# Kernel tuning notes

Hardware: AMD Instinct MI355X
Metric: run time of the kernel (lower is better)

## Reference

```python
import jax, jax.numpy as jnp
import numpy as np

B, S, D, H = 2, 2048, 1024, 16
DH = D // H  # 64


def setup_inputs() -> dict:
    key = jax.random.key(0)
    ks = jax.random.split(key, 6)
    scale = 1.0 / np.sqrt(D)
    x = jax.random.normal(ks[0], (B, S, D), dtype=jnp.float32)
    Wq = jax.random.normal(ks[1], (D, D), dtype=jnp.float32) * scale
    Wk = jax.random.normal(ks[2], (D, D), dtype=jnp.float32) * scale
    Wv = jax.random.normal(ks[3], (D, D), dtype=jnp.float32) * scale
    Wo = jax.random.normal(ks[4], (D, D), dtype=jnp.float32) * scale
    zeros = jnp.zeros((D,), dtype=jnp.float32)
    return {"x": x, "Wq": Wq, "bq": zeros, "Wk": Wk, "bk": zeros,
            "Wv": Wv, "bv": zeros, "Wo": Wo, "bo": zeros}


def reference(x, Wq, bq, Wk, bk, Wv, bv, Wo, bo):
    # x: [B, S, D]
    def split_heads(t):
        # [B, S, D] -> [B, H, S, DH]
        return t.reshape(B, S, H, DH).transpose(0, 2, 1, 3)

    q = split_heads(x @ Wq + bq)
    k = split_heads(x @ Wk + bk)
    v = split_heads(x @ Wv + bv)

    scores = jnp.einsum('bhqd,bhkd->bhqk', q, k) / jnp.sqrt(jnp.float32(DH))
    weights = jax.nn.softmax(scores, axis=-1)          # [B, H, S, S]
    o = jnp.einsum('bhqk,bhkd->bhqd', weights, v)       # [B, H, S, DH]
    o = o.transpose(0, 2, 1, 3).reshape(B, S, D)        # merge heads
    return o @ Wo + bo
```

## Files before the change

kernel.cpp:

```cpp
#include <hip/hip_runtime.h>
#include <hip/hip_bf16.h>

#define DEV __device__ __forceinline__

typedef short bf16x8 __attribute__((ext_vector_type(8)));
typedef float f32x4 __attribute__((ext_vector_type(4)));
typedef unsigned int u32;

constexpr int BB = 2, SS = 2048, DD = 1024, HH = 16, DHD = 64;
constexpr int MM = BB * SS;
#define QSC 0.1803368801111f

#if __has_builtin(__builtin_amdgcn_exp2f)
#define EXP2(x) __builtin_amdgcn_exp2f(x)
#else
#define EXP2(x) exp2f(x)
#endif

DEV unsigned short f2bf(float f) {
    union { float f; unsigned int u; } v; v.f = f;
    return (unsigned short)((v.u + 0x8000u) >> 16);
}
DEV u32 pk2bf(float a, float b) {
    union { float f; u32 u; } ua, ub; ua.f = a; ub.f = b;
    return ((ua.u + 0x8000u) >> 16) | ((ub.u + 0x8000u) & 0xffff0000u);
}

DEV bf16x8 ld_bf16x8(const unsigned short* p) { return *(const bf16x8*)p; }

DEV void gl16(const unsigned short* g, unsigned short* l) {
    __builtin_amdgcn_global_load_lds(
        (const __attribute__((address_space(1))) u32*)g,
        (__attribute__((address_space(3))) u32*)l, 16, 0, 0);
}

__global__ void x2bf(const float* __restrict__ x, unsigned short* __restrict__ xb) {
    int i = blockIdx.x * 256 + threadIdx.x;
    float4 v = ((const float4*)x)[i];
    uint2 o;
    o.x = pk2bf(v.x, v.y);
    o.y = pk2bf(v.z, v.w);
    ((uint2*)xb)[i] = o;
}

__global__ void transpose_w4(const float* __restrict__ W0, const float* __restrict__ W1,
                             const float* __restrict__ W2, const float* __restrict__ W3,
                             unsigned short* __restrict__ WtBase) {
    __shared__ float tile[32][33];
    const float* W = (blockIdx.z == 0) ? W0 : (blockIdx.z == 1) ? W1 : (blockIdx.z == 2) ? W2 : W3;
    unsigned short* Wt = WtBase + (size_t)blockIdx.z * DD * DD;
    int n0 = blockIdx.x * 32, k0 = blockIdx.y * 32;
    int tx = threadIdx.x, ty = threadIdx.y;
    #pragma unroll
    for (int i = 0; i < 4; ++i)
        tile[ty + 8 * i][tx] = W[(size_t)(k0 + ty + 8 * i) * DD + n0 + tx];
    __syncthreads();
    #pragma unroll
    for (int i = 0; i < 4; ++i)
        Wt[(size_t)(n0 + ty + 8 * i) * DD + k0 + tx] = f2bf(tile[tx][ty + 8 * i]);
}

__global__ __launch_bounds__(256) void qkv_gemm(
    const unsigned short* __restrict__ xb,
    const unsigned short* __restrict__ WtBase,
    const float* __restrict__ bq, const float* __restrict__ bk, const float* __restrict__ bv,
    unsigned short* __restrict__ Qb, unsigned short* __restrict__ Kb, unsigned short* __restrict__ Vt)
{
    __shared__ __align__(16) unsigned short Ald[2][128 * 32];
    __shared__ __align__(16) unsigned short Bld[2][128 * 32];

    const int z = blockIdx.z;
    const unsigned short* Wt = WtBase + (size_t)z * DD * DD;
    const float* bias = (z == 0) ? bq : (z == 1) ? bk : bv;

    const int m0g = blockIdx.y * 128;
    const int n0g = blockIdx.x * 128;
    const int wave = threadIdx.x >> 6, lane = threadIdx.x & 63;
    const int quad = lane >> 4, lcol = lane & 15;
    const int mb = (wave & 1) * 64, nb = (wave >> 1) * 64;

    f32x4 acc[4][4];
    #pragma unroll
    for (int i = 0; i < 4; ++i)
        #pragma unroll
        for (int j = 0; j < 4; ++j) acc[i][j] = (f32x4){0.f, 0.f, 0.f, 0.f};

    auto stage = [&](int ks, int bf) {
        #pragma unroll
        for (int i = 0; i < 4; ++i) {
            int j = wave * 4 + i;
            if (j < 8) {
                int bi = j * 64 + lane;
                int row = bi >> 2, p = (bi & 3) ^ (row & 3);
                gl16(xb + (size_t)(m0g + row) * DD + ks + p * 8, &Ald[bf][j * 512]);
            } else {
                int jj = j - 8;
                int bi = jj * 64 + lane;
                int row = bi >> 2, p = (bi & 3) ^ (row & 3);
                gl16(Wt + (size_t)(n0g + row) * DD + ks + p * 8, &Bld[bf][jj * 512]);
            }
        }
    };

    stage(0, 0);
    __syncthreads();

    for (int kk = 0; kk < 32; ++kk) {
        int bf = kk & 1;
        if (kk + 1 < 32) stage((kk + 1) * 32, (kk + 1) & 1);
        bf16x8 af[4], bfr[4];
        #pragma unroll
        for (int mt = 0; mt < 4; ++mt) {
            int row = mb + mt * 16 + lcol;
            af[mt] = ld_bf16x8(&Ald[bf][(row * 4 + (quad ^ (row & 3))) * 8]);
        }
        #pragma unroll
        for (int nt = 0; nt < 4; ++nt) {
            int row = nb + nt * 16 + lcol;
            bfr[nt] = ld_bf16x8(&Bld[bf][(row * 4 + (quad ^ (row & 3))) * 8]);
        }
        if (z < 2) {
            #pragma unroll
            for (int mt = 0; mt < 4; ++mt)
                #pragma unroll
                for (int nt = 0; nt < 4; ++nt)
                    acc[mt][nt] = __builtin_amdgcn_mfma_f32_16x16x32_bf16(bfr[nt], af[mt], acc[mt][nt], 0, 0, 0);
        } else {
            #pragma unroll
            for (int mt = 0; mt < 4; ++mt)
                #pragma unroll
                for (int nt = 0; nt < 4; ++nt)
                    acc[mt][nt] = __builtin_amdgcn_mfma_f32_16x16x32_bf16(af[mt], bfr[nt], acc[mt][nt], 0, 0, 0);
        }
        __syncthreads();
    }

    if (z < 2) {
        unsigned short* dst = (z == 0) ? Qb : Kb;
        const float sc = (z == 0) ? QSC : 1.0f;
        #pragma unroll
        for (int mt = 0; mt < 4; ++mt)
            #pragma unroll
            for (int nt = 0; nt < 4; ++nt) {
                int m = m0g + mb + mt * 16 + lcol;
                int nbt = n0g + nb + nt * 16 + quad * 4;
                int b = m >> 11, s = m & (SS - 1);
                int h = nbt >> 6, dh0 = nbt & 63;
                float4 bv4 = *(const float4*)&bias[nbt];
                uint2 o;
                o.x = pk2bf((acc[mt][nt][0] + bv4.x) * sc, (acc[mt][nt][1] + bv4.y) * sc);
                o.y = pk2bf((acc[mt][nt][2] + bv4.z) * sc, (acc[mt][nt][3] + bv4.w) * sc);
                *(uint2*)&dst[(((size_t)b * HH + h) * SS + s) * DHD + dh0] = o;
            }
    } else {
        #pragma unroll
        for (int mt = 0; mt < 4; ++mt)
            #pragma unroll
            for (int nt = 0; nt < 4; ++nt) {
                int n = n0g + nb + nt * 16 + lcol;
                int mbt = m0g + mb + mt * 16 + quad * 4;
                int h = n >> 6, dh = n & 63;
                int b = mbt >> 11, s0 = mbt & (SS - 1);
                float bvv = bias[n];
                uint2 o;
                o.x = pk2bf(acc[mt][nt][0] + bvv, acc[mt][nt][1] + bvv);
                o.y = pk2bf(acc[mt][nt][2] + bvv, acc[mt][nt][3] + bvv);
                *(uint2*)&Vt[(((size_t)b * HH + h) * DHD + dh) * SS + s0] = o;
            }
    }
}

__global__ __launch_bounds__(256) void attn(
    const unsigned short* __restrict__ Qb,
    const unsigned short* __restrict__ Kb,
    const unsigned short* __restrict__ Vt,
    unsigned short* __restrict__ Ob)
{
    __shared__ __align__(16) unsigned short Kld[2][64 * 64];
    __shared__ __align__(16) unsigned short Vld[2][64 * 64];
    __shared__ __align__(16) unsigned short tb[4][2][16 * 72];

    const int qt = blockIdx.x;
    const int bh = blockIdx.y;
    const int b = bh >> 4, h = bh & (HH - 1);
    const unsigned short* Qbh = Qb + (size_t)bh * SS * DHD;
    const unsigned short* Kbh = Kb + (size_t)bh * SS * DHD;
    const unsigned short* Vbh = Vt + (size_t)bh * DHD * SS;

    const int wave = threadIdx.x >> 6, lane = threadIdx.x & 63;
    const int quad = lane >> 4, lcol = lane & 15;
    const int rowbase = qt * 128 + wave * 32;

    bf16x8 qf[2][2];
    #pragma unroll
    for (int mt = 0; mt < 2; ++mt)
        #pragma unroll
        for (int kf = 0; kf < 2; ++kf)
            qf[mt][kf] = ld_bf16x8(Qbh + (size_t)(rowbase + mt * 16 + lcol) * DHD + kf * 32 + quad * 8);

    auto stage = [&](int c, int bf) {
        int kb = c * 64;
        #pragma unroll
        for (int i = 0; i < 4; ++i) {
            int j = wave * 4 + i;
            if (j < 8) {
                int bi = j * 64 + lane;
                int r = bi >> 3, p = (bi & 7) ^ (r & 7);
                gl16(Kbh + (size_t)(kb + r) * DHD + p * 8, &Kld[bf][j * 512]);
            } else {
                int jj = j - 8;
                int bi = jj * 64 + lane;
                int dh = bi >> 3, p = (bi & 7) ^ (dh & 7);
                gl16(Vbh + (size_t)dh * SS + kb + p * 8, &Vld[bf][jj * 512]);
            }
        }
    };

    stage(0, 0);
    __syncthreads();

    float m0 = -1e30f;
    #pragma unroll
    for (int kt = 0; kt < 4; ++kt) {
        int r0 = kt * 16 + lcol;
        bf16x8 ka0 = ld_bf16x8(&Kld[0][(r0 * 8 + (quad ^ (r0 & 7))) * 8]);
        bf16x8 ka1 = ld_bf16x8(&Kld[0][(r0 * 8 + ((quad + 4) ^ (r0 & 7))) * 8]);
        #pragma unroll
        for (int mt = 0; mt < 2; ++mt) {
            f32x4 s = (f32x4){0.f, 0.f, 0.f, 0.f};
            s = __builtin_amdgcn_mfma_f32_16x16x32_bf16(ka0, qf[mt][0], s, 0, 0, 0);
            s = __builtin_amdgcn_mfma_f32_16x16x32_bf16(ka1, qf[mt][1], s, 0, 0, 0);
            #pragma unroll
            for (int r = 0; r < 4; ++r) m0 = fmaxf(m0, s[r]);
        }
    }
    #pragma unroll
    for (int msk = 1; msk < 64; msk <<= 1) m0 = fmaxf(m0, __shfl_xor(m0, msk, 64));

    f32x4 oacc[2][4];
    #pragma unroll
    for (int mt = 0; mt < 2; ++mt)
        #pragma unroll
        for (int nt = 0; nt < 4; ++nt) oacc[mt][nt] = (f32x4){0.f, 0.f, 0.f, 0.f};
    float ps[2] = {0.f, 0.f};

    for (int c = 0; c < 32; ++c) {
        int bf = c & 1;
        if (c + 1 < 32) stage(c + 1, (c + 1) & 1);

        #pragma unroll
        for (int kt = 0; kt < 4; ++kt) {
            int r0 = kt * 16 + lcol;
            bf16x8 ka0 = ld_bf16x8(&Kld[bf][(r0 * 8 + (quad ^ (r0 & 7))) * 8]);
            bf16x8 ka1 = ld_bf16x8(&Kld[bf][(r0 * 8 + ((quad + 4) ^ (r0 & 7))) * 8]);
            #pragma unroll
            for (int mt = 0; mt < 2; ++mt) {
                f32x4 s = (f32x4){0.f, 0.f, 0.f, 0.f};
                s = __builtin_amdgcn_mfma_f32_16x16x32_bf16(ka0, qf[mt][0], s, 0, 0, 0);
                s = __builtin_amdgcn_mfma_f32_16x16x32_bf16(ka1, qf[mt][1], s, 0, 0, 0);
                float e0 = EXP2(s[0] - m0), e1 = EXP2(s[1] - m0);
                float e2 = EXP2(s[2] - m0), e3 = EXP2(s[3] - m0);
                ps[mt] += (e0 + e1) + (e2 + e3);
                *(uint2*)&tb[wave][mt][lcol * 72 + kt * 16 + quad * 4] =
                    make_uint2(pk2bf(e0, e1), pk2bf(e2, e3));
            }
        }

        #pragma unroll
        for (int kf2 = 0; kf2 < 2; ++kf2) {
            bf16x8 vb[4];
            #pragma unroll
            for (int nt = 0; nt < 4; ++nt) {
                int dh = nt * 16 + lcol;
                vb[nt] = ld_bf16x8(&Vld[bf][(dh * 8 + ((kf2 * 4 + quad) ^ (dh & 7))) * 8]);
            }
            #pragma unroll
            for (int mt = 0; mt < 2; ++mt) {
                bf16x8 pa = *(const bf16x8*)&tb[wave][mt][lcol * 72 + kf2 * 32 + quad * 8];
                #pragma unroll
                for (int nt = 0; nt < 4; ++nt)
                    oacc[mt][nt] = __builtin_amdgcn_mfma_f32_16x16x32_bf16(pa, vb[nt], oacc[mt][nt], 0, 0, 0);
            }
        }
        __syncthreads();
    }

    #pragma unroll
    for (int mt = 0; mt < 2; ++mt) {
        ps[mt] += __shfl_xor(ps[mt], 16, 64);
        ps[mt] += __shfl_xor(ps[mt], 32, 64);
    }
    float inv[2] = {1.0f / ps[0], 1.0f / ps[1]};
    #pragma unroll
    for (int mt = 0; mt < 2; ++mt)
        #pragma unroll
        for (int r = 0; r < 4; ++r) {
            float iv = __shfl(inv[mt], quad * 4 + r, 64);
            int srow = rowbase + mt * 16 + quad * 4 + r;
            size_t base = (((size_t)b * SS + srow) * HH + h) * DHD;
            #pragma unroll
            for (int nt = 0; nt < 4; ++nt)
                Ob[base + nt * 16 + lcol] = f2bf(oacc[mt][nt][r] * iv);
        }
}

__global__ __launch_bounds__(256) void out_gemm(
    const unsigned short* __restrict__ Ob,
    const unsigned short* __restrict__ Wto,
    const float* __restrict__ bo,
    float* __restrict__ out)
{
    __shared__ __align__(16) unsigned short Ald[2][128 * 32];
    __shared__ __align__(16) unsigned short Bld[2][128 * 32];

    const int m0g = blockIdx.y * 128;
    const int n0g = blockIdx.x * 128;
    const int wave = threadIdx.x >> 6, lane = threadIdx.x & 63;
    const int quad = lane >> 4, lcol = lane & 15;
    const int mb = (wave & 1) * 64, nb = (wave >> 1) * 64;

    f32x4 acc[4][4];
    #pragma unroll
    for (int i = 0; i < 4; ++i)
        #pragma unroll
        for (int j = 0; j < 4; ++j) acc[i][j] = (f32x4){0.f, 0.f, 0.f, 0.f};

    auto stage = [&](int ks, int bf) {
        #pragma unroll
        for (int i = 0; i < 4; ++i) {
            int j = wave * 4 + i;
            if (j < 8) {
                int bi = j * 64 + lane;
                int row = bi >> 2, p = (bi & 3) ^ (row & 3);
                gl16(Ob + (size_t)(m0g + row) * DD + ks + p * 8, &Ald[bf][j * 512]);
            } else {
                int jj = j - 8;
                int bi = jj * 64 + lane;
                int row = bi >> 2, p = (bi & 3) ^ (row & 3);
                gl16(Wto + (size_t)(n0g + row) * DD + ks + p * 8, &Bld[bf][jj * 512]);
            }
        }
    };

    stage(0, 0);
    __syncthreads();

    for (int kk = 0; kk < 32; ++kk) {
        int bf = kk & 1;
        if (kk + 1 < 32) stage((kk + 1) * 32, (kk + 1) & 1);
        bf16x8 af[4], bfr[4];
        #pragma unroll
        for (int mt = 0; mt < 4; ++mt) {
            int row = mb + mt * 16 + lcol;
            af[mt] = ld_bf16x8(&Ald[bf][(row * 4 + (quad ^ (row & 3))) * 8]);
        }
        #pragma unroll
        for (int nt = 0; nt < 4; ++nt) {
            int row = nb + nt * 16 + lcol;
            bfr[nt] = ld_bf16x8(&Bld[bf][(row * 4 + (quad ^ (row & 3))) * 8]);
        }
        #pragma unroll
        for (int mt = 0; mt < 4; ++mt)
            #pragma unroll
            for (int nt = 0; nt < 4; ++nt)
                acc[mt][nt] = __builtin_amdgcn_mfma_f32_16x16x32_bf16(af[mt], bfr[nt], acc[mt][nt], 0, 0, 0);
        __syncthreads();
    }

    #pragma unroll
    for (int mt = 0; mt < 4; ++mt)
        #pragma unroll
        for (int nt = 0; nt < 4; ++nt) {
            int n = n0g + nb + nt * 16 + lcol;
            float bv_ = bo[n];
            #pragma unroll
            for (int r = 0; r < 4; ++r) {
                int m = m0g + mb + mt * 16 + quad * 4 + r;
                out[(size_t)m * DD + n] = acc[mt][nt][r] + bv_;
            }
        }
}

extern "C" void kernel_launch(void* const* d_in, const int* in_sizes, int n_in,
                              void* d_out, int out_size, void* d_ws, size_t ws_size,
                              hipStream_t stream)
{
    const float* x  = (const float*)d_in[0];
    const float* Wq = (const float*)d_in[1];
    const float* bq = (const float*)d_in[2];
    const float* Wk = (const float*)d_in[3];
    const float* bk = (const float*)d_in[4];
    const float* Wv = (const float*)d_in[5];
    const float* bv = (const float*)d_in[6];
    const float* Wo = (const float*)d_in[7];
    const float* bo = (const float*)d_in[8];
    float* out = (float*)d_out;

    unsigned short* ws = (unsigned short*)d_ws;
    unsigned short* Wt  = ws;
    unsigned short* Wto = Wt + 3 * (size_t)DD * DD;
    unsigned short* Qb  = Wt + 4 * (size_t)DD * DD;
    unsigned short* Kb  = Qb + (size_t)MM * DD;
    unsigned short* Vt  = Kb + (size_t)MM * DD;
    unsigned short* xb  = Vt + (size_t)MM * DD;
    unsigned short* Ob  = xb;

    x2bf<<<MM * DD / 4 / 256, 256, 0, stream>>>(x, xb);
    transpose_w4<<<dim3(DD / 32, DD / 32, 4), dim3(32, 8), 0, stream>>>(Wq, Wk, Wv, Wo, Wt);

    qkv_gemm<<<dim3(DD / 128, MM / 128, 3), 256, 0, stream>>>(xb, Wt, bq, bk, bv, Qb, Kb, Vt);

    attn<<<dim3(SS / 128, BB * HH), 256, 0, stream>>>(Qb, Kb, Vt, Ob);

    out_gemm<<<dim3(DD / 128, MM / 128), 256, 0, stream>>>(Ob, Wto, bo, out);
}
```

Measured before the change: 221.4 us.

## Halve attention and output-GEMM tiles, swizzle block order, fold max into MFMA init

The attention kernel now gives each wave 16 query rows instead of 32, so the grid doubles to 1024 blocks, and it remaps block indices so that neighbouring blocks work on different batch-heads. The negative row max is preloaded into the MFMA accumulator, which removes the per-element subtract before exp2. bf16 packing now uses a single v_perm. The output GEMM tile is cut from 128x128 to 64x128 to launch more blocks. The intent is more parallelism and occupancy on the many CUs, in exchange for K/V being reloaded more often for each query row and less data reuse in the GEMM.

```diff
diff --git a/kernel.cpp b/kernel.cpp
--- a/kernel.cpp
+++ b/kernel.cpp
@@ -21,10 +21,17 @@
     union { float f; unsigned int u; } v; v.f = f;
     return (unsigned short)((v.u + 0x8000u) >> 16);
 }
+#if __has_builtin(__builtin_amdgcn_perm)
+DEV u32 pk2bf(float a, float b) {
+    union { float f; u32 u; } ua, ub; ua.f = a; ub.f = b;
+    return __builtin_amdgcn_perm(ub.u + 0x8000u, ua.u + 0x8000u, 0x07060302u);
+}
+#else
 DEV u32 pk2bf(float a, float b) {
     union { float f; u32 u; } ua, ub; ua.f = a; ub.f = b;
     return ((ua.u + 0x8000u) >> 16) | ((ub.u + 0x8000u) & 0xffff0000u);
 }
+#endif
 
 DEV bf16x8 ld_bf16x8(const unsigned short* p) { return *(const bf16x8*)p; }
 
@@ -178,10 +185,11 @@
 {
     __shared__ __align__(16) unsigned short Kld[2][64 * 64];
     __shared__ __align__(16) unsigned short Vld[2][64 * 64];
-    __shared__ __align__(16) unsigned short tb[4][2][16 * 72];
-
-    const int qt = blockIdx.x;
-    const int bh = blockIdx.y;
+    __shared__ __align__(16) unsigned short tb[4][16 * 68];
+
+    const int g = blockIdx.y * gridDim.x + blockIdx.x;
+    const int bh = (g & 7) * 4 + ((g >> 3) & 3);
+    const int qt = g >> 5;
     const int b = bh >> 4, h = bh & (HH - 1);
     const unsigned short* Qbh = Qb + (size_t)bh * SS * DHD;
     const unsigned short* Kbh = Kb + (size_t)bh * SS * DHD;
@@ -189,14 +197,10 @@
 
     const int wave = threadIdx.x >> 6, lane = threadIdx.x & 63;
     const int quad = lane >> 4, lcol = lane & 15;
-    const int rowbase = qt * 128 + wave * 32;
-
-    bf16x8 qf[2][2];
-    #pragma unroll
-    for (int mt = 0; mt < 2; ++mt)
-        #pragma unroll
-        for (int kf = 0; kf < 2; ++kf)
-            qf[mt][kf] = ld_bf16x8(Qbh + (size_t)(rowbase + mt * 16 + lcol) * DHD + kf * 32 + quad * 8);
+    const int rowbase = qt * 64 + wave * 16;
+
+    bf16x8 qf0 = ld_bf16x8(Qbh + (size_t)(rowbase + lcol) * DHD + quad * 8);
+    bf16x8 qf1 = ld_bf16x8(Qbh + (size_t)(rowbase + lcol) * DHD + 32 + quad * 8);
 
     auto stage = [&](int c, int bf) {
         int kb = c * 64;
@@ -225,24 +229,20 @@
         int r0 = kt * 16 + lcol;
         bf16x8 ka0 = ld_bf16x8(&Kld[0][(r0 * 8 + (quad ^ (r0 & 7))) * 8]);
         bf16x8 ka1 = ld_bf16x8(&Kld[0][(r0 * 8 + ((quad + 4) ^ (r0 & 7))) * 8]);
-        #pragma unroll
-        for (int mt = 0; mt < 2; ++mt) {
-            f32x4 s = (f32x4){0.f, 0.f, 0.f, 0.f};
-            s = __builtin_amdgcn_mfma_f32_16x16x32_bf16(ka0, qf[mt][0], s, 0, 0, 0);
-            s = __builtin_amdgcn_mfma_f32_16x16x32_bf16(ka1, qf[mt][1], s, 0, 0, 0);
-            #pragma unroll
-            for (int r = 0; r < 4; ++r) m0 = fmaxf(m0, s[r]);
-        }
+        f32x4 s = (f32x4){0.f, 0.f, 0.f, 0.f};
+        s = __builtin_amdgcn_mfma_f32_16x16x32_bf16(ka0, qf0, s, 0, 0, 0);
+        s = __builtin_amdgcn_mfma_f32_16x16x32_bf16(ka1, qf1, s, 0, 0, 0);
+        #pragma unroll
+        for (int r = 0; r < 4; ++r) m0 = fmaxf(m0, s[r]);
     }
     #pragma unroll
     for (int msk = 1; msk < 64; msk <<= 1) m0 = fmaxf(m0, __shfl_xor(m0, msk, 64));
-
-    f32x4 oacc[2][4];
-    #pragma unroll
-    for (int mt = 0; mt < 2; ++mt)
-        #pragma unroll
-        for (int nt = 0; nt < 4; ++nt) oacc[mt][nt] = (f32x4){0.f, 0.f, 0.f, 0.f};
-    float ps[2] = {0.f, 0.f};
+    const f32x4 minit = (f32x4){-m0, -m0, -m0, -m0};
+
+    f32x4 oacc[4];
+    #pragma unroll
+    for (int nt = 0; nt < 4; ++nt) oacc[nt] = (f32x4){0.f, 0.f, 0.f, 0.f};
+    float ps = 0.f;
 
     for (int c = 0; c < 32; ++c) {
         int bf = c & 1;
@@ -253,55 +253,41 @@
             int r0 = kt * 16 + lcol;
             bf16x8 ka0 = ld_bf16x8(&Kld[bf][(r0 * 8 + (quad ^ (r0 & 7))) * 8]);
             bf16x8 ka1 = ld_bf16x8(&Kld[bf][(r0 * 8 + ((quad + 4) ^ (r0 & 7))) * 8]);
-            #pragma unroll
-            for (int mt = 0; mt < 2; ++mt) {
-                f32x4 s = (f32x4){0.f, 0.f, 0.f, 0.f};
-                s = __builtin_amdgcn_mfma_f32_16x16x32_bf16(ka0, qf[mt][0], s, 0, 0, 0);
-                s = __builtin_amdgcn_mfma_f32_16x16x32_bf16(ka1, qf[mt][1], s, 0, 0, 0);
-                float e0 = EXP2(s[0] - m0), e1 = EXP2(s[1] - m0);
-                float e2 = EXP2(s[2] - m0), e3 = EXP2(s[3] - m0);
-                ps[mt] += (e0 + e1) + (e2 + e3);
-                *(uint2*)&tb[wave][mt][lcol * 72 + kt * 16 + quad * 4] =
-                    make_uint2(pk2bf(e0, e1), pk2bf(e2, e3));
-            }
+            f32x4 s = minit;
+            s = __builtin_amdgcn_mfma_f32_16x16x32_bf16(ka0, qf0, s, 0, 0, 0);
+            s = __builtin_amdgcn_mfma_f32_16x16x32_bf16(ka1, qf1, s, 0, 0, 0);
+            float e0 = EXP2(s[0]), e1 = EXP2(s[1]);
+            float e2 = EXP2(s[2]), e3 = EXP2(s[3]);
+            ps += (e0 + e1) + (e2 + e3);
+            *(uint2*)&tb[wave][lcol * 68 + kt * 16 + quad * 4] =
+                make_uint2(pk2bf(e0, e1), pk2bf(e2, e3));
         }
 
         #pragma unroll
         for (int kf2 = 0; kf2 < 2; ++kf2) {
-            bf16x8 vb[4];
+            bf16x8 pa = *(const bf16x8*)&tb[wave][lcol * 68 + kf2 * 32 + quad * 8];
             #pragma unroll
             for (int nt = 0; nt < 4; ++nt) {
                 int dh = nt * 16 + lcol;
-                vb[nt] = ld_bf16x8(&Vld[bf][(dh * 8 + ((kf2 * 4 + quad) ^ (dh & 7))) * 8]);
-            }
-            #pragma unroll
-            for (int mt = 0; mt < 2; ++mt) {
-                bf16x8 pa = *(const bf16x8*)&tb[wave][mt][lcol * 72 + kf2 * 32 + quad * 8];
-                #pragma unroll
-                for (int nt = 0; nt < 4; ++nt)
-                    oacc[mt][nt] = __builtin_amdgcn_mfma_f32_16x16x32_bf16(pa, vb[nt], oacc[mt][nt], 0, 0, 0);
+                bf16x8 vb = ld_bf16x8(&Vld[bf][(dh * 8 + ((kf2 * 4 + quad) ^ (dh & 7))) * 8]);
+                oacc[nt] = __builtin_amdgcn_mfma_f32_16x16x32_bf16(pa, vb, oacc[nt], 0, 0, 0);
             }
         }
         __syncthreads();
     }
 
-    #pragma unroll
-    for (int mt = 0; mt < 2; ++mt) {
-        ps[mt] += __shfl_xor(ps[mt], 16, 64);
-        ps[mt] += __shfl_xor(ps[mt], 32, 64);
-    }
-    float inv[2] = {1.0f / ps[0], 1.0f / ps[1]};
-    #pragma unroll
-    for (int mt = 0; mt < 2; ++mt)
-        #pragma unroll
-        for (int r = 0; r < 4; ++r) {
-            float iv = __shfl(inv[mt], quad * 4 + r, 64);
-            int srow = rowbase + mt * 16 + quad * 4 + r;
-            size_t base = (((size_t)b * SS + srow) * HH + h) * DHD;
-            #pragma unroll
-            for (int nt = 0; nt < 4; ++nt)
-                Ob[base + nt * 16 + lcol] = f2bf(oacc[mt][nt][r] * iv);
-        }
+    ps += __shfl_xor(ps, 16, 64);
+    ps += __shfl_xor(ps, 32, 64);
+    float inv = 1.0f / ps;
+    #pragma unroll
+    for (int r = 0; r < 4; ++r) {
+        float iv = __shfl(inv, quad * 4 + r, 64);
+        int srow = rowbase + quad * 4 + r;
+        size_t base = (((size_t)b * SS + srow) * HH + h) * DHD;
+        #pragma unroll
+        for (int nt = 0; nt < 4; ++nt)
+            Ob[base + nt * 16 + lcol] = f2bf(oacc[nt][r] * iv);
+    }
 }
 
 __global__ __launch_bounds__(256) void out_gemm(
@@ -310,31 +296,31 @@
     const float* __restrict__ bo,
     float* __restrict__ out)
 {
-    __shared__ __align__(16) unsigned short Ald[2][128 * 32];
+    __shared__ __align__(16) unsigned short Ald[2][64 * 32];
     __shared__ __align__(16) unsigned short Bld[2][128 * 32];
 
-    const int m0g = blockIdx.y * 128;
+    const int m0g = blockIdx.y * 64;
     const int n0g = blockIdx.x * 128;
     const int wave = threadIdx.x >> 6, lane = threadIdx.x & 63;
     const int quad = lane >> 4, lcol = lane & 15;
-    const int mb = (wave & 1) * 64, nb = (wave >> 1) * 64;
-
-    f32x4 acc[4][4];
+    const int nb = wave * 32;
+
+    f32x4 acc[4][2];
     #pragma unroll
     for (int i = 0; i < 4; ++i)
         #pragma unroll
-        for (int j = 0; j < 4; ++j) acc[i][j] = (f32x4){0.f, 0.f, 0.f, 0.f};
+        for (int j = 0; j < 2; ++j) acc[i][j] = (f32x4){0.f, 0.f, 0.f, 0.f};
 
     auto stage = [&](int ks, int bf) {
         #pragma unroll
-        for (int i = 0; i < 4; ++i) {
-            int j = wave * 4 + i;
-            if (j < 8) {
+        for (int i = 0; i < 3; ++i) {
+            int j = wave * 3 + i;
+            if (j < 4) {
                 int bi = j * 64 + lane;
                 int row = bi >> 2, p = (bi & 3) ^ (row & 3);
                 gl16(Ob + (size_t)(m0g + row) * DD + ks + p * 8, &Ald[bf][j * 512]);
             } else {
-                int jj = j - 8;
+                int jj = j - 4;
                 int bi = jj * 64 + lane;
                 int row = bi >> 2, p = (bi & 3) ^ (row & 3);
                 gl16(Wto + (size_t)(n0g + row) * DD + ks + p * 8, &Bld[bf][jj * 512]);
@@ -348,21 +334,21 @@
     for (int kk = 0; kk < 32; ++kk) {
         int bf = kk & 1;
         if (kk + 1 < 32) stage((kk + 1) * 32, (kk + 1) & 1);
-        bf16x8 af[4], bfr[4];
+        bf16x8 af[4], bfr[2];
         #pragma unroll
         for (int mt = 0; mt < 4; ++mt) {
-            int row = mb + mt * 16 + lcol;
+            int row = mt * 16 + lcol;
             af[mt] = ld_bf16x8(&Ald[bf][(row * 4 + (quad ^ (row & 3))) * 8]);
         }
         #pragma unroll
-        for (int nt = 0; nt < 4; ++nt) {
+        for (int nt = 0; nt < 2; ++nt) {
             int row = nb + nt * 16 + lcol;
             bfr[nt] = ld_bf16x8(&Bld[bf][(row * 4 + (quad ^ (row & 3))) * 8]);
         }
         #pragma unroll
         for (int mt = 0; mt < 4; ++mt)
             #pragma unroll
-            for (int nt = 0; nt < 4; ++nt)
+            for (int nt = 0; nt < 2; ++nt)
                 acc[mt][nt] = __builtin_amdgcn_mfma_f32_16x16x32_bf16(af[mt], bfr[nt], acc[mt][nt], 0, 0, 0);
         __syncthreads();
     }
@@ -370,12 +356,12 @@
     #pragma unroll
     for (int mt = 0; mt < 4; ++mt)
         #pragma unroll
-        for (int nt = 0; nt < 4; ++nt) {
+        for (int nt = 0; nt < 2; ++nt) {
             int n = n0g + nb + nt * 16 + lcol;
             float bv_ = bo[n];
             #pragma unroll
             for (int r = 0; r < 4; ++r) {
-                int m = m0g + mb + mt * 16 + quad * 4 + r;
+                int m = m0g + mt * 16 + quad * 4 + r;
                 out[(size_t)m * DD + n] = acc[mt][nt][r] + bv_;
             }
         }
@@ -410,7 +396,7 @@
 
     qkv_gemm<<<dim3(DD / 128, MM / 128, 3), 256, 0, stream>>>(xb, Wt, bq, bk, bv, Qb, Kb, Vt);
 
-    attn<<<dim3(SS / 128, BB * HH), 256, 0, stream>>>(Qb, Kb, Vt, Ob);
-
-    out_gemm<<<dim3(DD / 128, MM / 128), 256, 0, stream>>>(Ob, Wto, bo, out);
-}
+    attn<<<dim3(32, 32), 256, 0, stream>>>(Qb, Kb, Vt, Ob);
+
+    out_gemm<<<dim3(DD / 128, MM / 64), 256, 0, stream>>>(Ob, Wto, bo, out);
+}
```

Result: slower. 230.6 us (+4.2%).
